# Kernel tuning notes

Hardware: AMD Instinct MI355X
Metric: run time of the kernel (lower is better)

Reference implementation:

```python
import jax, jax.numpy as jnp
import numpy as np


def _greens(x, k0_raw, amp_raw):
    """Faithful TunableGreens: FFT-domain filtering with per-channel-pair Green's fn.
    NOTE: the source applies fftn over axes (0,1) (batch+H) but ifftn over axes (1,2)
    (H+W); we replicate that exactly."""
    H, W = x.shape[1], x.shape[2]
    k0 = jax.nn.softplus(k0_raw)    # (C, Co, 1, 1)
    amp = jax.nn.softplus(amp_raw)  # (C, Co, 1, 1)
    fy = (2.0 * jnp.pi) * jnp.fft.fftfreq(H, d=1.0).astype(jnp.float32)
    fx = (2.0 * jnp.pi) * jnp.fft.fftfreq(W, d=1.0).astype(jnp.float32)
    p = fy[:, None] ** 2 + fx[None, :] ** 2            # (H, W) = sum(freq_grid**2, -1)
    g_fourier = 1.0 / (amp * p - k0 - 1j)              # (C, Co, H, W) complex64
    u_fft = jnp.fft.fftn(x, axes=(0, 1))               # axes (0,1) as in source
    u_filtered = jnp.einsum('bijc,coij->bijo', u_fft, g_fourier)
    return jnp.fft.ifftn(u_filtered, axes=(1, 2)).real


def _D(Wm, x):
    # per-pixel channel mixing: x [b,i,j,c], Wm [b,i,j,c,o]
    return jnp.einsum('bijc,bijco->bijo', x, Wm)


def _project(k, W1, b1, W2, b2, W3, b3):
    act = lambda z: jnp.exp(-z ** 2)
    x = act(k @ W1 + b1)
    x = act(x @ W2 + b2)
    return x @ W3 + b3


def setup_inputs() -> dict:
    key = jax.random.key(0)
    ks = jax.random.split(key, 10)
    B, H, W, C = 2, 128, 128, 32
    d = {}
    d['u'] = jax.random.normal(ks[0], (B, H, W, C), jnp.float32)
    d['k'] = jax.random.normal(ks[1], (B, H, W, 1), jnp.float32)
    for i, n in enumerate(['g1', 'g2', 'g3', 'g4']):
        d[n] = jax.random.normal(ks[2 + i], (B, H, W, C, C), jnp.float32) * 0.1
    # Project MLP params (lecun-normal-ish scaling)
    d['W1'] = jax.random.normal(ks[6], (1, C), jnp.float32)
    d['b1'] = jnp.zeros((C,), jnp.float32)
    d['W2'] = jax.random.normal(ks[7], (C, C), jnp.float32) * (1.0 / np.sqrt(C))
    d['b2'] = jnp.zeros((C,), jnp.float32)
    d['W3'] = jax.random.normal(ks[8], (C, C), jnp.float32) * (1.0 / np.sqrt(C))
    d['b3'] = jnp.zeros((C,), jnp.float32)
    # TunableGreens params, constant(1.0) init as in source
    d['k0_G'] = jnp.ones((C, C, 1, 1), jnp.float32)
    d['amp_G'] = jnp.ones((C, C, 1, 1), jnp.float32)
    d['k0_Gs'] = jnp.ones((C, C, 1, 1), jnp.float32)
    d['amp_Gs'] = jnp.ones((C, C, 1, 1), jnp.float32)
    return d


def reference(u, k, g1, g2, g3, g4, W1, b1, W2, b2, W3, b3,
              k0_G, amp_G, k0_Gs, amp_Gs):
    s = _project(k, W1, b1, W2, b2, W3, b3)           # [B,H,W,C]
    u1 = _D(g4, _greens(s, k0_Gs, amp_Gs))
    u2 = _D(g1, _greens(_D(g2, u), k0_G, amp_G)) + _D(g3, u)
    return u1 + u2
```

## Files before the change

kernel.cpp:

```cpp
#include <hip/hip_runtime.h>

using u16 = unsigned short;
using u32 = unsigned int;

#define PI2 6.283185307179586f

struct cpx { float x, y; };

typedef unsigned int uvec4 __attribute__((ext_vector_type(4)));
typedef float fvec4 __attribute__((ext_vector_type(4)));

__device__ __forceinline__ uint4 ldnt_u4(const uint4* p){
  uvec4 v = __builtin_nontemporal_load((const uvec4*)p);
  uint4 r; r.x = v.x; r.y = v.y; r.z = v.z; r.w = v.w; return r;
}
__device__ __forceinline__ float4 ldnt_f4(const float4* p){
  fvec4 v = __builtin_nontemporal_load((const fvec4*)p);
  float4 r; r.x = v.x; r.y = v.y; r.z = v.z; r.w = v.w; return r;
}

__device__ __forceinline__ float bf2f(u16 h){ return __uint_as_float(((u32)h) << 16); }
__device__ __forceinline__ u16 f2bf(float f){
  u32 u = __float_as_uint(f);
  u = u + 0x7fffu + ((u >> 16) & 1u);
  return (u16)(u >> 16);
}

__device__ __forceinline__ float ldv(const void* base, size_t i, int md){
  return md ? ((const float*)base)[i] : bf2f(((const u16*)base)[i]);
}

__device__ __forceinline__ cpx cadd(cpx a, cpx b){ return {a.x+b.x, a.y+b.y}; }
__device__ __forceinline__ cpx csub(cpx a, cpx b){ return {a.x-b.x, a.y-b.y}; }
__device__ __forceinline__ cpx cmul(cpx a, cpx b){ return {a.x*b.x - a.y*b.y, a.x*b.y + a.y*b.x}; }
__device__ __forceinline__ int br6(int l){ return (int)(__brev((u32)l) >> 26); }
__device__ __forceinline__ cpx shflx(cpx v, int m){
  cpx r; r.x = __shfl_xor(v.x, m, 64); r.y = __shfl_xor(v.y, m, 64); return r;
}

__device__ __forceinline__ void make_tw(int l, cpx tw[6]){
  #pragma unroll
  for (int s = 0; s < 6; s++){
    int h = 64 >> s;
    float ang = -PI2 * (float)(l & (h-1)) / (float)(2*h);
    float sv, cv; sincosf(ang, &sv, &cv);
    tw[s] = {cv, sv};
  }
}

__device__ __forceinline__ void fft_fwd(cpx& v0, cpx& v1, int l, const cpx tw[6]){
  cpx a = cadd(v0, v1), b = csub(v0, v1);
  v0 = a; v1 = cmul(b, tw[0]);
  #pragma unroll
  for (int s = 1; s < 6; s++){
    int h = 64 >> s;
    cpx p0 = shflx(v0, h), p1 = shflx(v1, h);
    bool up = (l & h) != 0;
    cpx n0 = up ? cmul(csub(p0, v0), tw[s]) : cadd(v0, p0);
    cpx n1 = up ? cmul(csub(p1, v1), tw[s]) : cadd(v1, p1);
    v0 = n0; v1 = n1;
  }
  { cpx p0 = shflx(v0, 1), p1 = shflx(v1, 1);
    bool up = (l & 1) != 0;
    v0 = up ? csub(p0, v0) : cadd(v0, p0);
    v1 = up ? csub(p1, v1) : cadd(v1, p1); }
}

__device__ __forceinline__ void fft_inv(cpx& v0, cpx& v1, int l, const cpx tw[6]){
  { cpx p0 = shflx(v0, 1), p1 = shflx(v1, 1);
    bool up = (l & 1) != 0;
    v0 = up ? csub(p0, v0) : cadd(v0, p0);
    v1 = up ? csub(p1, v1) : cadd(v1, p1); }
  #pragma unroll
  for (int s = 5; s >= 1; s--){
    int h = 64 >> s;
    cpx twc = {tw[s].x, -tw[s].y};
    cpx p0 = shflx(v0, h), p1 = shflx(v1, h);
    bool up = (l & h) != 0;
    cpx t0 = cmul(up ? v0 : p0, twc);
    cpx t1 = cmul(up ? v1 : p1, twc);
    v0 = up ? csub(p0, t0) : cadd(v0, t0);
    v1 = up ? csub(p1, t1) : cadd(v1, t1);
  }
  { cpx twc = {tw[0].x, -tw[0].y};
    cpx t = cmul(v1, twc);
    cpx n0 = cadd(v0, t), n1 = csub(v0, t);
    v0 = n0; v1 = n1; }
}

__device__ __forceinline__ float softplusf(float x){ return (x > 20.0f) ? x : log1pf(expf(x)); }

__device__ __forceinline__ void acc8_bf(uint4 a, uint4 b, float x0, float x1, float acc[8]){
  acc[0] = fmaf(x0, __uint_as_float(a.x << 16),         acc[0]);
  acc[1] = fmaf(x0, __uint_as_float(a.x & 0xffff0000u), acc[1]);
  acc[2] = fmaf(x0, __uint_as_float(a.y << 16),         acc[2]);
  acc[3] = fmaf(x0, __uint_as_float(a.y & 0xffff0000u), acc[3]);
  acc[4] = fmaf(x0, __uint_as_float(a.z << 16),         acc[4]);
  acc[5] = fmaf(x0, __uint_as_float(a.z & 0xffff0000u), acc[5]);
  acc[6] = fmaf(x0, __uint_as_float(a.w << 16),         acc[6]);
  acc[7] = fmaf(x0, __uint_as_float(a.w & 0xffff0000u), acc[7]);
  acc[0] = fmaf(x1, __uint_as_float(b.x << 16),         acc[0]);
  acc[1] = fmaf(x1, __uint_as_float(b.x & 0xffff0000u), acc[1]);
  acc[2] = fmaf(x1, __uint_as_float(b.y << 16),         acc[2]);
  acc[3] = fmaf(x1, __uint_as_float(b.y & 0xffff0000u), acc[3]);
  acc[4] = fmaf(x1, __uint_as_float(b.z << 16),         acc[4]);
  acc[5] = fmaf(x1, __uint_as_float(b.z & 0xffff0000u), acc[5]);
  acc[6] = fmaf(x1, __uint_as_float(b.w << 16),         acc[6]);
  acc[7] = fmaf(x1, __uint_as_float(b.w & 0xffff0000u), acc[7]);
}
__device__ __forceinline__ void acc8_f32(float4 a0, float4 a1, float4 b0, float4 b1,
                                         float x0, float x1, float acc[8]){
  acc[0] = fmaf(x0, a0.x, acc[0]); acc[1] = fmaf(x0, a0.y, acc[1]);
  acc[2] = fmaf(x0, a0.z, acc[2]); acc[3] = fmaf(x0, a0.w, acc[3]);
  acc[4] = fmaf(x0, a1.x, acc[4]); acc[5] = fmaf(x0, a1.y, acc[5]);
  acc[6] = fmaf(x0, a1.z, acc[6]); acc[7] = fmaf(x0, a1.w, acc[7]);
  acc[0] = fmaf(x1, b0.x, acc[0]); acc[1] = fmaf(x1, b0.y, acc[1]);
  acc[2] = fmaf(x1, b0.z, acc[2]); acc[3] = fmaf(x1, b0.w, acc[3]);
  acc[4] = fmaf(x1, b1.x, acc[4]); acc[5] = fmaf(x1, b1.y, acc[5]);
  acc[6] = fmaf(x1, b1.z, acc[6]); acc[7] = fmaf(x1, b1.w, acc[7]);
}

__global__ void k_detect(const void* g1, int* flag){
  __shared__ int cnt;
  if (threadIdx.x == 0) cnt = 0;
  __syncthreads();
  const u16* p = (const u16*)g1;
  int local = 0;
  for (int i = threadIdx.x; i < 4096; i += 256){
    float v = bf2f(p[i]);
    if (!(fabsf(v) < 100.0f)) local++;
  }
  atomicAdd(&cnt, local);
  __syncthreads();
  if (threadIdx.x == 0) *flag = (cnt > 64) ? 1 : 0;
}

__global__ void k_tabs(const void* k0G, const void* ampG, const void* k0Gs, const void* ampGs,
                       float* tabs, const int* flag){
  int md = *flag;
  for (int i = threadIdx.x; i < 1024; i += 256){
    tabs[i]        = softplusf(ldv(ampGs, i, md));
    tabs[1024 + i] = softplusf(ldv(k0Gs, i, md));
    tabs[2048 + i] = softplusf(ldv(ampG, i, md));
    tabs[3072 + i] = softplusf(ldv(k0G, i, md));
  }
}

__global__ __launch_bounds__(256) void k_project(const void* kin, const void* W1, const void* b1,
    const void* W2, const void* b2, const void* W3, const void* b3, float* S, const int* flag){
  __shared__ float sW2[1024], sW3[1024], sml[128];
  int md = *flag;
  int t = threadIdx.x;
  for (int i = t; i < 1024; i += 256){ sW2[i] = ldv(W2, i, md); sW3[i] = ldv(W3, i, md); }
  if (t < 32){
    sml[t]     = ldv(W1, t, md); sml[32+t] = ldv(b1, t, md);
    sml[64+t]  = ldv(b2, t, md); sml[96+t] = ldv(b3, t, md);
  }
  __syncthreads();
  int pix = blockIdx.x * 256 + t;
  float kv = ldv(kin, pix, md);
  float a1[32], a2[32];
  #pragma unroll
  for (int c = 0; c < 32; c++){ float z = fmaf(kv, sml[c], sml[32+c]); a1[c] = expf(-z*z); }
  for (int o = 0; o < 32; o++){
    float z = sml[64+o];
    #pragma unroll
    for (int c = 0; c < 32; c++) z = fmaf(a1[c], sW2[c*32+o], z);
    a2[o] = expf(-z*z);
  }
  for (int o = 0; o < 32; o++){
    float sv = sml[96+o];
    #pragma unroll
    for (int c = 0; c < 32; c++) sv = fmaf(a2[c], sW3[c*32+o], sv);
    S[(size_t)pix*32 + o] = sv;
  }
}

__global__ __launch_bounds__(256) void k_dmat(const void* u, const void* g2, float* D, const int* flag){
  int md = *flag;
  int t = threadIdx.x, l = t & 63;
  size_t pix = (size_t)blockIdx.x * 8 + (size_t)(t >> 6) * 2;
  int c32 = l & 31, ch = l >> 2;
  float xa = ldv(u, pix*32 + c32, md);
  float xb = ldv(u, (pix+1)*32 + c32, md);
  float acc0[8] = {0.f,0.f,0.f,0.f,0.f,0.f,0.f,0.f};
  float acc1[8] = {0.f,0.f,0.f,0.f,0.f,0.f,0.f,0.f};
  if (md){
    const float4* Ra = (const float4*)((const float*)g2 + pix*1024);
    const float4* Rb = (const float4*)((const float*)g2 + (pix+1)*1024);
    float4 aa = ldnt_f4(Ra+2*l), ab = ldnt_f4(Ra+2*l+1), ac = ldnt_f4(Ra+128+2*l), ad = ldnt_f4(Ra+128+2*l+1);
    float4 ba = ldnt_f4(Rb+2*l), bb = ldnt_f4(Rb+2*l+1), bc = ldnt_f4(Rb+128+2*l), bd = ldnt_f4(Rb+128+2*l+1);
    float xa0 = __shfl(xa, ch, 64), xa1 = __shfl(xa, 16+ch, 64);
    float xb0 = __shfl(xb, ch, 64), xb1 = __shfl(xb, 16+ch, 64);
    acc8_f32(aa, ab, ac, ad, xa0, xa1, acc0);
    acc8_f32(ba, bb, bc, bd, xb0, xb1, acc1);
  } else {
    const uint4* Ra = (const uint4*)((const u16*)g2 + pix*1024);
    const uint4* Rb = (const uint4*)((const u16*)g2 + (pix+1)*1024);
    uint4 a0 = ldnt_u4(Ra+l), a1 = ldnt_u4(Ra+64+l);
    uint4 b0 = ldnt_u4(Rb+l), b1 = ldnt_u4(Rb+64+l);
    float xa0 = __shfl(xa, ch, 64), xa1 = __shfl(xa, 16+ch, 64);
    float xb0 = __shfl(xb, ch, 64), xb1 = __shfl(xb, 16+ch, 64);
    acc8_bf(a0, a1, xa0, xa1, acc0);
    acc8_bf(b0, b1, xb0, xb1, acc1);
  }
  #pragma unroll
  for (int d = 4; d <= 32; d <<= 1){
    #pragma unroll
    for (int jj = 0; jj < 8; jj++){
      acc0[jj] += __shfl_xor(acc0[jj], d, 64);
      acc1[jj] += __shfl_xor(acc1[jj], d, 64);
    }
  }
  if (l < 4){
    ((float4*)(D + pix*32))[2*l]       = make_float4(acc0[0], acc0[1], acc0[2], acc0[3]);
    ((float4*)(D + pix*32))[2*l+1]     = make_float4(acc0[4], acc0[5], acc0[6], acc0[7]);
    ((float4*)(D + (pix+1)*32))[2*l]   = make_float4(acc1[0], acc1[1], acc1[2], acc1[3]);
    ((float4*)(D + (pix+1)*32))[2*l+1] = make_float4(acc1[4], acc1[5], acc1[6], acc1[7]);
  }
}

__global__ __launch_bounds__(512) void kg_a(const float* S, const float* Dd, const float* tabs, float2* Q){
  __shared__ __align__(16) cpx E[64*128];
  int t = threadIdx.x;
  int p = blockIdx.x >> 7, j = blockIdx.x & 127;
  const float* X = p ? Dd : S;
  const float* ampT = tabs + p*2048;
  const float* k0T  = ampT + 1024;
  int l = t & 63, w = t >> 6;
  cpx tw[6]; make_tw(l, tw);

  {
    int h = t >> 2, ch = (t & 3) * 8;
    const float4* x0 = (const float4*)(X + (((size_t)h)*128 + j)*32 + ch);
    const float4* x1 = (const float4*)(X + (((size_t)(128 + h))*128 + j)*32 + ch);
    #pragma unroll
    for (int q = 0; q < 2; q++){
      float4 A = x0[q], B = x1[q];
      int c = ch + q*4;
      E[(c+0)*128 + h] = {A.x+B.x, 0.f};  E[(32+c+0)*128 + h] = {A.x-B.x, 0.f};
      E[(c+1)*128 + h] = {A.y+B.y, 0.f};  E[(32+c+1)*128 + h] = {A.y-B.y, 0.f};
      E[(c+2)*128 + h] = {A.z+B.z, 0.f};  E[(32+c+2)*128 + h] = {A.z-B.z, 0.f};
      E[(c+3)*128 + h] = {A.w+B.w, 0.f};  E[(32+c+3)*128 + h] = {A.w-B.w, 0.f};
    }
  }
  __syncthreads();
  for (int c = w; c < 64; c += 8){
    cpx* col = E + c*128;
    cpx v0 = col[l], v1 = col[l+64];
    fft_fwd(v0, v1, l, tw);
    ((float4*)col)[br6(l)] = make_float4(v0.x, v0.y, v1.x, v1.y);
  }
  __syncthreads();
  {
    int o = t & 31, ig = t >> 5;
    float aT[32], kT[32];
    #pragma unroll
    for (int c = 0; c < 32; c++){ aT[c] = ampT[c*32+o]; kT[c] = k0T[c*32+o]; }
    float fj = (j < 64) ? (float)j : (float)(j - 128);
    fj *= (PI2 / 128.0f);
    float px = fj * fj;
    for (int chunk = 0; chunk < 2; chunk++){
      cpx y0[4], y1[4];
      #pragma unroll
      for (int q = 0; q < 4; q++){
        int i = ig + 16*(chunk*4 + q);
        float fi = (i < 64) ? (float)i : (float)(i - 128);
        fi *= (PI2 / 128.0f);
        float pp = fmaf(fi, fi, px);
        cpx a0 = {0.f, 0.f}, a1 = {0.f, 0.f};
        #pragma unroll
        for (int c = 0; c < 32; c++){
          float dd  = fmaf(aT[c], pp, -kT[c]);
          float inv = __builtin_amdgcn_rcpf(fmaf(dd, dd, 1.0f));
          float gr = dd * inv, gi = inv;
          cpx x0 = E[c*128 + i];
          cpx x1 = E[(32+c)*128 + i];
          a0.x = fmaf(x0.x, gr, fmaf(-x0.y, gi, a0.x));
          a0.y = fmaf(x0.x, gi, fmaf( x0.y, gr, a0.y));
          a1.x = fmaf(x1.x, gr, fmaf(-x1.y, gi, a1.x));
          a1.y = fmaf(x1.x, gi, fmaf( x1.y, gr, a1.y));
        }
        y0[q] = a0; y1[q] = a1;
      }
      __syncthreads();
      #pragma unroll
      for (int q = 0; q < 4; q++){
        int i = ig + 16*(chunk*4 + q);
        E[o*128 + i]      = y0[q];
        E[(32+o)*128 + i] = y1[q];
      }
      __syncthreads();
    }
  }
  for (int cidx = w; cidx < 64; cidx += 8){
    cpx* col = E + cidx*128;
    float4 tv = ((const float4*)col)[br6(l)];
    cpx v0 = {tv.x, tv.y}, v1 = {tv.z, tv.w};
    fft_inv(v0, v1, l, tw);
    const float sc = 1.0f/128.0f;
    col[l]    = {v0.x*sc, v0.y*sc};
    col[l+64] = {v1.x*sc, v1.y*sc};
  }
  __syncthreads();
  {
    int o = t & 31, bb = (t >> 5) & 1, yb = t >> 6;
    for (int m = 0; m < 16; m++){
      int y = yb + 8*m;
      cpx v = E[(bb*32+o)*128 + y];
      Q[((((size_t)(p*2+bb))*128 + y)*128 + j)*32 + o] = make_float2(v.x, v.y);
    }
  }
}

#define ZS 130
#define RS 133
__global__ __launch_bounds__(256) void kg_c(const float2* Q, float* G0, float* G1){
  __shared__ __align__(16) cpx Z[32*ZS];
  __shared__ float R[32*RS];
  int t = threadIdx.x, l = t & 63, w = t >> 6;
  int idx = blockIdx.x;
  int p = idx >> 8, rem = idx & 255, bb = rem >> 7, y = rem & 127;
  cpx tw[6]; make_tw(l, tw);
  const float4* src = (const float4*)(Q + ((size_t)((p*2+bb)*128 + y))*4096);
  for (int q = t; q < 2048; q += 256){
    float4 v = src[q];
    int m = q*2, jj = m >> 5, c = m & 31;
    Z[c*ZS + jj]     = {v.x, v.y};
    Z[(c+1)*ZS + jj] = {v.z, v.w};
  }
  __syncthreads();
  for (int c = w; c < 32; c += 4){
    cpx* col = Z + c*ZS;
    float4 tv = ((const float4*)col)[br6(l)];
    cpx v0 = {tv.x, tv.y}, v1 = {tv.z, tv.w};
    fft_inv(v0, v1, l, tw);
    R[c*RS + l]      = v0.x * (1.0f/128.0f);
    R[c*RS + l + 64] = v1.x * (1.0f/128.0f);
  }
  __syncthreads();
  float* dst = (p ? G1 : G0) + ((size_t)(bb*128 + y))*4096;
  int jj = t >> 3, c4 = (t & 7)*4;
  for (int rep = 0; rep < 4; rep++){
    int j2 = jj + rep*32;
    float4 o4 = { R[(c4+0)*RS + j2], R[(c4+1)*RS + j2],
                  R[(c4+2)*RS + j2], R[(c4+3)*RS + j2] };
    ((float4*)(dst + (size_t)j2*32))[c4 >> 2] = o4;
  }
}

__global__ __launch_bounds__(256) void k_final(const void* u, const void* g1, const void* g3, const void* g4,
    const float* G0, const float* G1, void* out, const int* flag, int pix0){
  int md = *flag;
  int t = threadIdx.x, l = t & 63;
  size_t pix = (size_t)pix0 + (size_t)blockIdx.x * 4 + (t >> 6);
  int c32 = l & 31, ch = l >> 2;
  float xs = G0[pix*32 + c32];
  float xm = G1[pix*32 + c32];
  float xu = ldv(u, pix*32 + c32, md);
  float acc[8] = {0.f,0.f,0.f,0.f,0.f,0.f,0.f,0.f};
  if (md){
    const float4* R4 = (const float4*)((const float*)g4 + pix*1024);
    const float4* R1 = (const float4*)((const float*)g1 + pix*1024);
    const float4* R3 = (const float4*)((const float*)g3 + pix*1024);
    float4 p4a = R4[2*l], p4b = R4[2*l+1], q4a = R4[128+2*l], q4b = R4[128+2*l+1];
    float4 p1a = R1[2*l], p1b = R1[2*l+1], q1a = R1[128+2*l], q1b = R1[128+2*l+1];
    float4 p3a = ldnt_f4(R3+2*l), p3b = ldnt_f4(R3+2*l+1), q3a = ldnt_f4(R3+128+2*l), q3b = ldnt_f4(R3+128+2*l+1);
    float xs0 = __shfl(xs, ch, 64), xs1 = __shfl(xs, 16+ch, 64);
    float xm0 = __shfl(xm, ch, 64), xm1 = __shfl(xm, 16+ch, 64);
    float xu0 = __shfl(xu, ch, 64), xu1 = __shfl(xu, 16+ch, 64);
    acc8_f32(p4a, p4b, q4a, q4b, xs0, xs1, acc);
    acc8_f32(p1a, p1b, q1a, q1b, xm0, xm1, acc);
    acc8_f32(p3a, p3b, q3a, q3b, xu0, xu1, acc);
  } else {
    const uint4* R4 = (const uint4*)((const u16*)g4 + pix*1024);
    const uint4* R1 = (const uint4*)((const u16*)g1 + pix*1024);
    const uint4* R3 = (const uint4*)((const u16*)g3 + pix*1024);
    uint4 a4 = R4[l], b4 = R4[64+l];
    uint4 a1 = R1[l], b1 = R1[64+l];
    uint4 a3 = ldnt_u4(R3+l), b3 = ldnt_u4(R3+64+l);
    float xs0 = __shfl(xs, ch, 64), xs1 = __shfl(xs, 16+ch, 64);
    float xm0 = __shfl(xm, ch, 64), xm1 = __shfl(xm, 16+ch, 64);
    float xu0 = __shfl(xu, ch, 64), xu1 = __shfl(xu, 16+ch, 64);
    acc8_bf(a4, b4, xs0, xs1, acc);
    acc8_bf(a1, b1, xm0, xm1, acc);
    acc8_bf(a3, b3, xu0, xu1, acc);
  }
  #pragma unroll
  for (int d = 4; d <= 32; d <<= 1){
    #pragma unroll
    for (int jj = 0; jj < 8; jj++) acc[jj] += __shfl_xor(acc[jj], d, 64);
  }
  if (l < 4){
    if (md){
      float4 o0 = {acc[0], acc[1], acc[2], acc[3]};
      float4 o1 = {acc[4], acc[5], acc[6], acc[7]};
      ((float4*)out)[pix*8 + 2*l]     = o0;
      ((float4*)out)[pix*8 + 2*l + 1] = o1;
    } else {
      uint4 v;
      v.x = (u32)f2bf(acc[0]) | ((u32)f2bf(acc[1]) << 16);
      v.y = (u32)f2bf(acc[2]) | ((u32)f2bf(acc[3]) << 16);
      v.z = (u32)f2bf(acc[4]) | ((u32)f2bf(acc[5]) << 16);
      v.w = (u32)f2bf(acc[6]) | ((u32)f2bf(acc[7]) << 16);
      ((uint4*)out)[pix*4 + l] = v;
    }
  }
}

extern "C" void kernel_launch(void* const* d_in, const int* in_sizes, int n_in,
                              void* d_out, int out_size, void* d_ws, size_t ws_size,
                              hipStream_t stream){
  (void)in_sizes; (void)n_in; (void)out_size; (void)ws_size;
  const void* u    = d_in[0];
  const void* kk   = d_in[1];
  const void* g1   = d_in[2];
  const void* g2   = d_in[3];
  const void* g3   = d_in[4];
  const void* g4   = d_in[5];
  const void* W1   = d_in[6];
  const void* b1   = d_in[7];
  const void* W2   = d_in[8];
  const void* b2   = d_in[9];
  const void* W3   = d_in[10];
  const void* b3   = d_in[11];
  const void* k0G  = d_in[12];
  const void* ampG = d_in[13];
  const void* k0Gs = d_in[14];
  const void* ampGs= d_in[15];

  float* ws   = (float*)d_ws;
  float* S    = ws;
  float* Dd   = ws + (1u<<20);
  float2* Q   = (float2*)(ws + 2*(1u<<20));
  float* G0   = ws + 6*(1u<<20);
  float* G1b  = ws + 7*(1u<<20);
  float* tabs = ws + 8*(1u<<20);
  int*   flag = (int*)(tabs + 4096);

  k_detect <<<1,    256, 0, stream>>>(g1, flag);
  k_tabs   <<<1,    256, 0, stream>>>(k0G, ampG, k0Gs, ampGs, tabs, flag);
  k_project<<<128,  256, 0, stream>>>(kk, W1, b1, W2, b2, W3, b3, S, flag);
  k_dmat   <<<4096, 256, 0, stream>>>(u, g2, Dd, flag);
  kg_a     <<<256,  512, 0, stream>>>(S, Dd, tabs, Q);
  kg_c     <<<512,  256, 0, stream>>>(Q, G0, G1b);
  k_final  <<<4096, 256, 0, stream>>>(u, g1, g3, g4, G0, G1b, (void*)d_out, flag, 0);
  k_final  <<<4096, 256, 0, stream>>>(u, g1, g3, g4, G0, G1b, (void*)d_out, flag, 16384);
}
```

Baseline: 538.9 us.

## Split FFT-filter kernels across batch halves and channel halves for more blocks

kg_a now launches one 256-thread block per (pass, batch-frequency, column) instead of handling both batch frequency bins in a 512-thread block, which halves shared memory and the per-thread accumulators. kg_c is split by channel half, so each block does 16 inverse FFTs instead of 32. Both changes double the block count on the 256-CU GPU to improve occupancy and load balance. The cost is redundant loads of the input columns (each kg_a block reads both batch rows) and smaller, less coalesced writes in kg_c.

```diff
diff --git a/kernel.cpp b/kernel.cpp
--- a/kernel.cpp
+++ b/kernel.cpp
@@ -220,10 +220,12 @@
   }
 }
 
-__global__ __launch_bounds__(512) void kg_a(const float* S, const float* Dd, const float* tabs, float2* Q){
-  __shared__ __align__(16) cpx E[64*128];
+#define ES 130
+__global__ __launch_bounds__(256) void kg_a(const float* S, const float* Dd, const float* tabs, float2* Q){
+  __shared__ __align__(16) cpx E[32*ES];
   int t = threadIdx.x;
-  int p = blockIdx.x >> 7, j = blockIdx.x & 127;
+  int bid = blockIdx.x;
+  int p = bid >> 8, b = (bid >> 7) & 1, j = bid & 127;
   const float* X = p ? Dd : S;
   const float* ampT = tabs + p*2048;
   const float* k0T  = ampT + 1024;
@@ -231,22 +233,23 @@
   cpx tw[6]; make_tw(l, tw);
 
   {
-    int h = t >> 2, ch = (t & 3) * 8;
+    int h = t >> 1, ch = (t & 1) * 16;
     const float4* x0 = (const float4*)(X + (((size_t)h)*128 + j)*32 + ch);
     const float4* x1 = (const float4*)(X + (((size_t)(128 + h))*128 + j)*32 + ch);
-    #pragma unroll
-    for (int q = 0; q < 2; q++){
+    float sgn = b ? -1.f : 1.f;
+    #pragma unroll
+    for (int q = 0; q < 4; q++){
       float4 A = x0[q], B = x1[q];
       int c = ch + q*4;
-      E[(c+0)*128 + h] = {A.x+B.x, 0.f};  E[(32+c+0)*128 + h] = {A.x-B.x, 0.f};
-      E[(c+1)*128 + h] = {A.y+B.y, 0.f};  E[(32+c+1)*128 + h] = {A.y-B.y, 0.f};
-      E[(c+2)*128 + h] = {A.z+B.z, 0.f};  E[(32+c+2)*128 + h] = {A.z-B.z, 0.f};
-      E[(c+3)*128 + h] = {A.w+B.w, 0.f};  E[(32+c+3)*128 + h] = {A.w-B.w, 0.f};
+      E[(c+0)*ES + h] = {fmaf(sgn, B.x, A.x), 0.f};
+      E[(c+1)*ES + h] = {fmaf(sgn, B.y, A.y), 0.f};
+      E[(c+2)*ES + h] = {fmaf(sgn, B.z, A.z), 0.f};
+      E[(c+3)*ES + h] = {fmaf(sgn, B.w, A.w), 0.f};
     }
   }
   __syncthreads();
-  for (int c = w; c < 64; c += 8){
-    cpx* col = E + c*128;
+  for (int c = w; c < 32; c += 4){
+    cpx* col = E + c*ES;
     cpx v0 = col[l], v1 = col[l+64];
     fft_fwd(v0, v1, l, tw);
     ((float4*)col)[br6(l)] = make_float4(v0.x, v0.y, v1.x, v1.y);
@@ -260,41 +263,37 @@
     float fj = (j < 64) ? (float)j : (float)(j - 128);
     fj *= (PI2 / 128.0f);
     float px = fj * fj;
-    for (int chunk = 0; chunk < 2; chunk++){
-      cpx y0[4], y1[4];
+    for (int chunk = 0; chunk < 4; chunk++){
+      cpx y0[4];
       #pragma unroll
       for (int q = 0; q < 4; q++){
-        int i = ig + 16*(chunk*4 + q);
+        int i = ig + 8*(chunk*4 + q);
         float fi = (i < 64) ? (float)i : (float)(i - 128);
         fi *= (PI2 / 128.0f);
         float pp = fmaf(fi, fi, px);
-        cpx a0 = {0.f, 0.f}, a1 = {0.f, 0.f};
+        cpx a0 = {0.f, 0.f};
         #pragma unroll
         for (int c = 0; c < 32; c++){
           float dd  = fmaf(aT[c], pp, -kT[c]);
           float inv = __builtin_amdgcn_rcpf(fmaf(dd, dd, 1.0f));
           float gr = dd * inv, gi = inv;
-          cpx x0 = E[c*128 + i];
-          cpx x1 = E[(32+c)*128 + i];
+          cpx x0 = E[c*ES + i];
           a0.x = fmaf(x0.x, gr, fmaf(-x0.y, gi, a0.x));
           a0.y = fmaf(x0.x, gi, fmaf( x0.y, gr, a0.y));
-          a1.x = fmaf(x1.x, gr, fmaf(-x1.y, gi, a1.x));
-          a1.y = fmaf(x1.x, gi, fmaf( x1.y, gr, a1.y));
         }
-        y0[q] = a0; y1[q] = a1;
+        y0[q] = a0;
       }
       __syncthreads();
       #pragma unroll
       for (int q = 0; q < 4; q++){
-        int i = ig + 16*(chunk*4 + q);
-        E[o*128 + i]      = y0[q];
-        E[(32+o)*128 + i] = y1[q];
+        int i = ig + 8*(chunk*4 + q);
+        E[o*ES + i] = y0[q];
       }
       __syncthreads();
     }
   }
-  for (int cidx = w; cidx < 64; cidx += 8){
-    cpx* col = E + cidx*128;
+  for (int cidx = w; cidx < 32; cidx += 4){
+    cpx* col = E + cidx*ES;
     float4 tv = ((const float4*)col)[br6(l)];
     cpx v0 = {tv.x, tv.y}, v1 = {tv.z, tv.w};
     fft_inv(v0, v1, l, tw);
@@ -304,11 +303,11 @@
   }
   __syncthreads();
   {
-    int o = t & 31, bb = (t >> 5) & 1, yb = t >> 6;
+    int o = t & 31, yb = t >> 5;
     for (int m = 0; m < 16; m++){
       int y = yb + 8*m;
-      cpx v = E[(bb*32+o)*128 + y];
-      Q[((((size_t)(p*2+bb))*128 + y)*128 + j)*32 + o] = make_float2(v.x, v.y);
+      cpx v = E[o*ES + y];
+      Q[((((size_t)(p*2+b))*128 + y)*128 + j)*32 + o] = make_float2(v.x, v.y);
     }
   }
 }
@@ -316,36 +315,37 @@
 #define ZS 130
 #define RS 133
 __global__ __launch_bounds__(256) void kg_c(const float2* Q, float* G0, float* G1){
-  __shared__ __align__(16) cpx Z[32*ZS];
-  __shared__ float R[32*RS];
+  __shared__ __align__(16) cpx Z[16*ZS];
+  __shared__ float R[16*RS];
   int t = threadIdx.x, l = t & 63, w = t >> 6;
   int idx = blockIdx.x;
-  int p = idx >> 8, rem = idx & 255, bb = rem >> 7, y = rem & 127;
+  int p = idx >> 9, rem = idx & 511, bb = rem >> 8, y = (rem >> 1) & 127, h = rem & 1;
   cpx tw[6]; make_tw(l, tw);
   const float4* src = (const float4*)(Q + ((size_t)((p*2+bb)*128 + y))*4096);
-  for (int q = t; q < 2048; q += 256){
+  for (int i = t; i < 1024; i += 256){
+    int q = (i >> 3)*16 + 8*h + (i & 7);
     float4 v = src[q];
-    int m = q*2, jj = m >> 5, c = m & 31;
-    Z[c*ZS + jj]     = {v.x, v.y};
-    Z[(c+1)*ZS + jj] = {v.z, v.w};
-  }
-  __syncthreads();
-  for (int c = w; c < 32; c += 4){
-    cpx* col = Z + c*ZS;
+    int m = q*2, jj = m >> 5, cl = (m & 31) - 16*h;
+    Z[cl*ZS + jj]     = {v.x, v.y};
+    Z[(cl+1)*ZS + jj] = {v.z, v.w};
+  }
+  __syncthreads();
+  for (int cl = w; cl < 16; cl += 4){
+    cpx* col = Z + cl*ZS;
     float4 tv = ((const float4*)col)[br6(l)];
     cpx v0 = {tv.x, tv.y}, v1 = {tv.z, tv.w};
     fft_inv(v0, v1, l, tw);
-    R[c*RS + l]      = v0.x * (1.0f/128.0f);
-    R[c*RS + l + 64] = v1.x * (1.0f/128.0f);
+    R[cl*RS + l]      = v0.x * (1.0f/128.0f);
+    R[cl*RS + l + 64] = v1.x * (1.0f/128.0f);
   }
   __syncthreads();
   float* dst = (p ? G1 : G0) + ((size_t)(bb*128 + y))*4096;
-  int jj = t >> 3, c4 = (t & 7)*4;
-  for (int rep = 0; rep < 4; rep++){
-    int j2 = jj + rep*32;
+  int jj = t >> 2, c4 = (t & 3)*4;
+  for (int rep = 0; rep < 2; rep++){
+    int j2 = jj + rep*64;
     float4 o4 = { R[(c4+0)*RS + j2], R[(c4+1)*RS + j2],
                   R[(c4+2)*RS + j2], R[(c4+3)*RS + j2] };
-    ((float4*)(dst + (size_t)j2*32))[c4 >> 2] = o4;
+    ((float4*)(dst + (size_t)j2*32 + 16*h))[c4 >> 2] = o4;
   }
 }
 
@@ -442,8 +442,8 @@
   k_tabs   <<<1,    256, 0, stream>>>(k0G, ampG, k0Gs, ampGs, tabs, flag);
   k_project<<<128,  256, 0, stream>>>(kk, W1, b1, W2, b2, W3, b3, S, flag);
   k_dmat   <<<4096, 256, 0, stream>>>(u, g2, Dd, flag);
-  kg_a     <<<256,  512, 0, stream>>>(S, Dd, tabs, Q);
-  kg_c     <<<512,  256, 0, stream>>>(Q, G0, G1b);
+  kg_a     <<<512,  256, 0, stream>>>(S, Dd, tabs, Q);
+  kg_c     <<<1024, 256, 0, stream>>>(Q, G0, G1b);
   k_final  <<<4096, 256, 0, stream>>>(u, g1, g3, g4, G0, G1b, (void*)d_out, flag, 0);
   k_final  <<<4096, 256, 0, stream>>>(u, g1, g3, g4, G0, G1b, (void*)d_out, flag, 16384);
 }
```

Result: no change. 533.1 us (-1.1%).
